# Optimization experiments

Hardware: AMD Instinct MI355X
Metric: run time of the kernel (lower is better)

## Reference

```python
import jax, jax.numpy as jnp
import numpy as np

B, W, M = 16, 32, 512
NH, HALF, K, H = 64, 32, 8, 8
LK = W // 2               # long-conv kernel size
LOUT = W - 2 * (LK - 1)   # = 2 (dilated valid conv output length)
NSP = 10                  # n_spatial (hardcoded in module)
GC1_IN = (1 + LOUT) * K   # 24


def setup_inputs() -> dict:
    key = jax.random.key(0)
    ks = jax.random.split(key, 23)
    def n(k, shp, s=0.1):
        return jax.random.normal(k, shp, jnp.float32) * s
    return dict(
        x=jax.random.normal(ks[0], (B, W, M), jnp.float32),
        adj=jax.random.uniform(ks[1], (M, M), jnp.float32) / M,  # row-normalized-ish dense adj
        Wih=n(ks[2], (NH, 1)), Whh=n(ks[3], (NH, NH)),
        bih=n(ks[4], (NH,)), bhh=n(ks[5], (NH,)),
        W1=n(ks[6], (HALF, NH)), W2=n(ks[7], (HALF, NH)), b1=n(ks[8], (HALF,)),
        V=n(ks[9], (HALF,)), bv=n(ks[10], (1,)),
        Wb=n(ks[11], (M, M)), wb=n(ks[12], (1,)),
        conv_w=n(ks[13], (K, 1, W)), conv_b=n(ks[14], (K,)),
        convl_w=n(ks[15], (K, 1, LK)), convl_b=n(ks[16], (K,)),
        gc1_w=n(ks[17], (GC1_IN, NH)), gc1_b=n(ks[18], (NH,)),
        gc2_w=n(ks[19], (NH, NSP)), gc2_b=n(ks[20], (NSP,)),
        out_w=n(ks[21], (H, NSP + NH)), out_b=n(ks[22], (H,)),
    )


def reference(x, adj, Wih, Whh, bih, bhh, W1, W2, b1, V, bv, Wb, wb,
              conv_w, conv_b, convl_w, convl_b, gc1_w, gc1_b, gc2_w, gc2_b,
              out_w, out_b):
    b = x.shape[0]
    # [b, w, m] -> per-node sequences [b*m, w]
    seq = jnp.transpose(x, (0, 2, 1)).reshape(b * M, W)

    # vanilla tanh RNN, input_size=1 (batched over all b*m series)
    inp = seq[:, :, None] * Wih[:, 0] + (bih + bhh)          # [b*m, w, nh]
    def step(h, it):
        return jnp.tanh(it + h @ Whh.T), None
    h0 = jnp.zeros((b * M, NH), x.dtype)
    last_hid, _ = jax.lax.scan(step, h0, jnp.swapaxes(inp, 0, 1))
    last_hid = last_hid.reshape(b, M, NH)                    # out_temporal

    # pairwise additive attention: a[b,i,j] = V . elu(W1 h_j + W2 h_i + b1) + bv
    e1 = last_hid @ W1.T                                     # [b, m, half] (j role)
    e2 = last_hid @ W2.T                                     # [b, m, half] (i role)
    a = jax.nn.elu(e2[:, :, None, :] + e1[:, None, :, :] + b1)  # [b,m,m,half]
    a_mx = a @ V + bv                                        # [b, m, m]
    # F.normalize(p=2, dim=1)
    norm = jnp.sqrt(jnp.sum(a_mx * a_mx, axis=1, keepdims=True))
    a_mx = a_mx / jnp.maximum(norm, 1e-12)

    # per-node short conv (kernel == window -> out len 1) as a single matmul
    r_short = seq @ conv_w[:, 0, :].T + conv_b               # [b*m, k]
    # per-node dilated long conv, batched over all b*m series
    r_long = jax.lax.conv_general_dilated(
        seq[:, None, :], convl_w, window_strides=(1,), padding='VALID',
        rhs_dilation=(2,), dimension_numbers=('NCW', 'OIW', 'NCW'))
    r_long = r_long + convl_b[None, :, None]                 # [b*m, k, LOUT]
    r = jnp.concatenate([r_short[:, :, None], r_long], axis=-1)  # [b*m, k, 1+LOUT]
    r = jax.nn.relu(r.reshape(b, M, GC1_IN))

    # gated mix of static normalized adj and learned attention adj
    c = jax.nn.sigmoid(a_mx @ Wb + wb)
    adj_mix = adj[None] * c + a_mx * (1.0 - c)               # [b, m, m]

    # two dense graph conv layers: relu(adj @ (h @ W) + b)
    h1 = jax.nn.relu(adj_mix @ (r @ gc1_w) + gc1_b)          # [b, m, nh]
    out_spatial = jax.nn.relu(adj_mix @ (h1 @ gc2_w) + gc2_b)  # [b, m, nsp]

    feat = jnp.concatenate([out_spatial, last_hid], axis=-1)  # [b, m, nsp+nh]
    out = feat @ out_w.T + out_b                              # [b, m, h]
    return jnp.transpose(out, (0, 2, 1))                      # [b, h, m]
```

## Files before the change

### kernel.cpp

```cpp
#include <hip/hip_runtime.h>


typedef __attribute__((ext_vector_type(8))) short bf16x8;
typedef __attribute__((ext_vector_type(4))) float f32x4;
#define MFMA16 __builtin_amdgcn_mfma_f32_16x16x32_bf16

__device__ __forceinline__ unsigned short f2bf(float f) {
    unsigned u = __float_as_uint(f);
    u += 0x7fff + ((u >> 16) & 1);
    return (unsigned short)(u >> 16);
}
__device__ __forceinline__ float bf2f(unsigned short h) {
    return __uint_as_float(((unsigned)h) << 16);
}
__device__ __forceinline__ float fast_tanh(float x) {
    float e = __expf(2.f * x);
    return 1.f - 2.f / (e + 1.f);
}

__global__ __launch_bounds__(256) void fused1_kernel(
    const float* __restrict__ x, const float* __restrict__ Wih,
    const float* __restrict__ Whh, const float* __restrict__ bih,
    const float* __restrict__ bhh, const float* __restrict__ W1,
    const float* __restrict__ W2, float* __restrict__ lh,
    float* __restrict__ e1, float* __restrict__ e2,
    const float* __restrict__ conv_w, const float* __restrict__ conv_b,
    const float* __restrict__ convl_w, const float* __restrict__ convl_b,
    const float* __restrict__ gc1_w, unsigned short* __restrict__ rgT,
    const float* __restrict__ Wb, unsigned short* __restrict__ WbT,
    float* __restrict__ nrmss)
{
    __shared__ __align__(16) char smem[17408];
    int blk = blockIdx.x, t = threadIdx.x;

    if (blk < 128) {
        int wid = t >> 6, lane = t & 63;
        int l15 = lane & 15, quad = lane >> 4;
        int rowblk = blk * 64;
        int row0 = rowblk + wid * 16;
        int b = rowblk >> 9, mb = rowblk & 511;
        float* xs = (float*)smem;
        unsigned short* hs = (unsigned short*)(smem + 8192);

        bf16x8 afr[4][2];
#pragma unroll
        for (int mt = 0; mt < 4; ++mt)
#pragma unroll
            for (int hf = 0; hf < 2; ++hf) {
                const float* src = Whh + (16 * mt + l15) * 64 + 32 * hf + quad * 8;
                union { bf16x8 v; unsigned short u[8]; } tmp;
#pragma unroll
                for (int j = 0; j < 8; ++j) tmp.u[j] = f2bf(src[j]);
                afr[mt][hf] = tmp.v;
            }
        bf16x8 wfr[2][2][2];
#pragma unroll
        for (int e = 0; e < 2; ++e)
#pragma unroll
            for (int nt = 0; nt < 2; ++nt)
#pragma unroll
                for (int kf = 0; kf < 2; ++kf) {
                    const float* Wsrc = (e ? W2 : W1);
                    const float* src = Wsrc + (16 * nt + l15) * 64 + 32 * kf + quad * 8;
                    union { bf16x8 v; unsigned short u[8]; } tmp;
#pragma unroll
                    for (int j = 0; j < 8; ++j) tmp.u[j] = f2bf(src[j]);
                    wfr[e][nt][kf] = tmp.v;
                }
        float wihv[4][4], bsv[4][4];
#pragma unroll
        for (int mt = 0; mt < 4; ++mt)
#pragma unroll
            for (int r = 0; r < 4; ++r) {
                int n = 16 * mt + quad * 4 + r;
                wihv[mt][r] = Wih[n];
                bsv[mt][r]  = bih[n] + bhh[n];
            }

        for (int u = t; u < 2048; u += 256) {
            int tt = u >> 6, c = u & 63;
            xs[tt * 64 + c] = x[(b * 32 + tt) * 512 + mb + c];
        }
        for (int u = lane; u < 1152; u += 64) hs[wid * 1152 + u] = 0;
        __syncthreads();

        int mloc = wid * 16;
        unsigned short* hw0 = hs + wid * 1152;
        float th[4][4];
        for (int tstep = 0; tstep < 32; ++tstep) {
            bf16x8 b0 = *(bf16x8*)(hw0 + l15 * 72 + quad * 8);
            bf16x8 b1 = *(bf16x8*)(hw0 + l15 * 72 + 32 + quad * 8);
            float xt = xs[tstep * 64 + mloc + l15];
            f32x4 acc[4];
#pragma unroll
            for (int mt = 0; mt < 4; ++mt) {
                f32x4 z = {0.f, 0.f, 0.f, 0.f};
                acc[mt] = MFMA16(afr[mt][0], b0, z, 0, 0, 0);
                acc[mt] = MFMA16(afr[mt][1], b1, acc[mt], 0, 0, 0);
            }
#pragma unroll
            for (int mt = 0; mt < 4; ++mt) {
                ushort4 hwv;
#pragma unroll
                for (int r = 0; r < 4; ++r)
                    th[mt][r] = fast_tanh(acc[mt][r] + xt * wihv[mt][r] + bsv[mt][r]);
                hwv.x = f2bf(th[mt][0]); hwv.y = f2bf(th[mt][1]);
                hwv.z = f2bf(th[mt][2]); hwv.w = f2bf(th[mt][3]);
                *(ushort4*)(hw0 + l15 * 72 + 16 * mt + quad * 4) = hwv;
            }
        }
#pragma unroll
        for (int mt = 0; mt < 4; ++mt)
            *(float4*)(lh + (row0 + l15) * 64 + 16 * mt + quad * 4) =
                make_float4(th[mt][0], th[mt][1], th[mt][2], th[mt][3]);

        bf16x8 a0 = *(bf16x8*)(hw0 + l15 * 72 + quad * 8);
        bf16x8 a1 = *(bf16x8*)(hw0 + l15 * 72 + 32 + quad * 8);
#pragma unroll
        for (int e = 0; e < 2; ++e) {
            float* dst = e ? e2 : e1;
#pragma unroll
            for (int nt = 0; nt < 2; ++nt) {
                f32x4 z = {0.f, 0.f, 0.f, 0.f};
                f32x4 ee = MFMA16(a0, wfr[e][nt][0], z, 0, 0, 0);
                ee = MFMA16(a1, wfr[e][nt][1], ee, 0, 0, 0);
#pragma unroll
                for (int r = 0; r < 4; ++r)
                    dst[(row0 + quad * 4 + r) * 32 + 16 * nt + l15] = ee[r];
            }
        }
    } else if (blk < 384) {
        int blk2 = blk - 128;
        int r0 = blk2 * 32;
        int bb = r0 >> 9, m0 = r0 & 511;
        float* xs  = (float*)smem;
        float* rrs = (float*)(smem + 4096);
        for (int u = t; u < 1024; u += 256) {
            int w = u >> 5, mm = u & 31;
            xs[u] = x[(bb * 32 + w) * 512 + m0 + mm];
        }
        __syncthreads();
        {
            int k = t & 7, rl = t >> 3;
            float s = conv_b[k];
            for (int w = 0; w < 32; ++w) s += xs[w * 32 + rl] * conv_w[k * 32 + w];
            float l0 = convl_b[k], l1 = l0;
            for (int tt = 0; tt < 16; ++tt) {
                float wv = convl_w[k * 16 + tt];
                l0 += xs[(2 * tt) * 32 + rl] * wv;
                l1 += xs[(2 * tt + 1) * 32 + rl] * wv;
            }
            rrs[rl * 25 + k * 3 + 0] = fmaxf(s, 0.f);
            rrs[rl * 25 + k * 3 + 1] = fmaxf(l0, 0.f);
            rrs[rl * 25 + k * 3 + 2] = fmaxf(l1, 0.f);
        }
        __syncthreads();
        int rl = t & 31, nb = t >> 5;
#pragma unroll
        for (int q = 0; q < 8; ++q) {
            int n = nb * 8 + q;
            float acc = 0.f;
#pragma unroll
            for (int c = 0; c < 24; ++c) acc += rrs[rl * 25 + c] * gc1_w[c * 64 + n];
            rgT[bb * 32768 + n * 512 + m0 + rl] = f2bf(acc);
        }
    } else if (blk < 640) {
        int bid = blk - 384;
        int nb = (bid & 15) * 32, kb = (bid >> 4) * 32;
        float* tile = (float*)smem;
        for (int u = t; u < 1024; u += 256) {
            int r = u >> 5, c = u & 31;
            tile[r * 33 + c] = Wb[(kb + r) * 512 + nb + c];
        }
        __syncthreads();
        for (int u = t; u < 1024; u += 256) {
            int r = u >> 5, c = u & 31;
            WbT[(nb + r) * 512 + kb + c] = f2bf(tile[c * 33 + r]);
        }
    } else {
        nrmss[(blk - 640) * 256 + t] = 0.f;
    }
}

__global__ __launch_bounds__(256) void amx_kernel(
    const float* __restrict__ e1, const float* __restrict__ e2,
    const float* __restrict__ b1p, const float* __restrict__ Vp,
    const float* __restrict__ bvp, unsigned short* __restrict__ amxb,
    float* __restrict__ nrmss)
{
    int bb = blockIdx.z;
    int i0 = blockIdx.y * 64, j0 = blockIdx.x * 64;
    __shared__ float e2s[64][33], e1s[64][33];
    __shared__ float Vs[32];
    __shared__ float red[16][68];
    int t = threadIdx.x;
    for (int u = t; u < 2048; u += 256) {
        int r = u >> 5, c = u & 31;
        e2s[r][c] = e2[(bb * 512 + i0 + r) * 32 + c];
        e1s[r][c] = e1[(bb * 512 + j0 + r) * 32 + c] + b1p[c];
    }
    if (t < 32) Vs[t] = Vp[t];
    __syncthreads();
    int ti = (t >> 4) * 4, tj = (t & 15) * 4;
    float acc[4][4] = {};
#pragma unroll
    for (int h = 0; h < 32; ++h) {
        float vv = Vs[h];
        float xi[4], yj[4], Exi[4], Eyj[4];
#pragma unroll
        for (int p = 0; p < 4; ++p) { xi[p] = e2s[ti + p][h]; Exi[p] = __expf(xi[p]); }
#pragma unroll
        for (int q = 0; q < 4; ++q) { yj[q] = e1s[tj + q][h]; Eyj[q] = __expf(yj[q]); }
#pragma unroll
        for (int p = 0; p < 4; ++p)
#pragma unroll
            for (int q = 0; q < 4; ++q) {
                float v = xi[p] + yj[q];
                float prod = Exi[p] * Eyj[q];
                float el = v > 0.f ? v : prod - 1.f;
                acc[p][q] += vv * el;
            }
    }
    float bv = bvp[0];
    float ss[4] = {0.f, 0.f, 0.f, 0.f};
#pragma unroll
    for (int p = 0; p < 4; ++p) {
        float v0 = acc[p][0] + bv, v1 = acc[p][1] + bv;
        float v2 = acc[p][2] + bv, v3 = acc[p][3] + bv;
        ushort4 o;
        o.x = f2bf(v0); o.y = f2bf(v1); o.z = f2bf(v2); o.w = f2bf(v3);
        *(ushort4*)(amxb + (bb * 512 + i0 + ti + p) * 512 + j0 + tj) = o;
        ss[0] += v0 * v0; ss[1] += v1 * v1; ss[2] += v2 * v2; ss[3] += v3 * v3;
    }
#pragma unroll
    for (int q = 0; q < 4; ++q) red[t >> 4][tj + q] = ss[q];
    __syncthreads();
    if (t < 64) {
        float s = 0.f;
#pragma unroll
        for (int g = 0; g < 16; ++g) s += red[g][t];
        atomicAdd(&nrmss[bb * 512 + j0 + t], s);
    }
}

__global__ __launch_bounds__(256) void gemm_adjmix(
    const unsigned short* __restrict__ amxb, const unsigned short* __restrict__ WbT,
    const float* __restrict__ wbp, const float* __restrict__ adj,
    const float* __restrict__ nrmss, unsigned short* __restrict__ adjmix)
{
    int bb = blockIdx.z;
    int i0 = blockIdx.y * 64, j0 = blockIdx.x * 64;
    __shared__ __align__(16) short As[64 * 72];
    __shared__ __align__(16) short Bs[64 * 72];
    __shared__ float rn[512];
    int t = threadIdx.x, w = t >> 6, lane = t & 63;
    int l15 = lane & 15, quad = lane >> 4;
    for (int u = t; u < 512; u += 256)
        rn[u] = 1.f / fmaxf(sqrtf(nrmss[bb * 512 + u]), 1e-12f);
    const unsigned short* Ag = amxb + bb * 262144;
    f32x4 acc[4] = {};
    for (int kk = 1; kk <= 8; ++kk) {
        int k0 = (j0 + 64 * kk) & 511;
        __syncthreads();
#pragma unroll
        for (int u0 = 0; u0 < 2; ++u0) {
            int u = t + u0 * 256;
            int i = u >> 3, o = u & 7;
            *(int4*)(Bs + i * 72 + o * 8) =
                *(const int4*)(WbT + (j0 + i) * 512 + k0 + o * 8);
            union { int4 v; unsigned short us[8]; } ur;
            ur.v = *(const int4*)(Ag + (i0 + i) * 512 + k0 + o * 8);
            union { int4 v; unsigned short us[8]; } ow;
#pragma unroll
            for (int c = 0; c < 8; ++c)
                ow.us[c] = f2bf(bf2f(ur.us[c]) * rn[k0 + o * 8 + c]);
            *(int4*)(As + i * 72 + o * 8) = ow.v;
        }
        __syncthreads();
        bf16x8 a0 = *(bf16x8*)(As + (16 * w + l15) * 72 + quad * 8);
        bf16x8 a1 = *(bf16x8*)(As + (16 * w + l15) * 72 + 32 + quad * 8);
#pragma unroll
        for (int nt = 0; nt < 4; ++nt) {
            bf16x8 b0 = *(bf16x8*)(Bs + (16 * nt + l15) * 72 + quad * 8);
            bf16x8 b1 = *(bf16x8*)(Bs + (16 * nt + l15) * 72 + 32 + quad * 8);
            acc[nt] = MFMA16(a0, b0, acc[nt], 0, 0, 0);
            acc[nt] = MFMA16(a1, b1, acc[nt], 0, 0, 0);
        }
    }
    float wb = wbp[0];
#pragma unroll
    for (int nt = 0; nt < 4; ++nt)
#pragma unroll
    for (int r = 0; r < 4; ++r) {
        int il = 16 * w + quad * 4 + r;
        int jl = 16 * nt + l15;
        int i = i0 + il, j = j0 + jl;
        float s  = acc[nt][r] + wb;
        float cv = 1.f / (1.f + __expf(-s));
        float am = bf2f((unsigned short)As[il * 72 + jl]);
        float ad = adj[i * 512 + j];
        adjmix[(bb * 512 + i) * 512 + j] = f2bf(ad * cv + am * (1.f - cv));
    }
}

__global__ __launch_bounds__(256) void gemm_h1(
    const unsigned short* __restrict__ adjmix, const unsigned short* __restrict__ rgT,
    const float* __restrict__ gc1_b, const float* __restrict__ gc2_w,
    float* __restrict__ h1g)
{
    int bb = blockIdx.y;
    int i0 = blockIdx.x * 32;
    __shared__ __align__(16) short As[32 * 72];
    __shared__ __align__(16) short Bs[64 * 72];
    __shared__ float h1s[32][72];
    int t = threadIdx.x, w = t >> 6, lane = t & 63;
    int l15 = lane & 15, quad = lane >> 4;
    int rt = w & 1, ntb = (w >> 1) * 2;
    const unsigned short* Ag = adjmix + bb * 262144;
    const unsigned short* Bg = rgT + bb * 32768;
    f32x4 acc[2] = {};
    for (int k0 = 0; k0 < 512; k0 += 64) {
        __syncthreads();
        {
            int i = t >> 3, o = t & 7;
            *(int4*)(As + i * 72 + o * 8) =
                *(const int4*)(Ag + (i0 + i) * 512 + k0 + o * 8);
        }
#pragma unroll
        for (int u0 = 0; u0 < 2; ++u0) {
            int u = t + u0 * 256;
            int i = u >> 3, o = u & 7;
            *(int4*)(Bs + i * 72 + o * 8) =
                *(const int4*)(Bg + i * 512 + k0 + o * 8);
        }
        __syncthreads();
        bf16x8 a0 = *(bf16x8*)(As + (16 * rt + l15) * 72 + quad * 8);
        bf16x8 a1 = *(bf16x8*)(As + (16 * rt + l15) * 72 + 32 + quad * 8);
#pragma unroll
        for (int q = 0; q < 2; ++q) {
            int nt = ntb + q;
            bf16x8 b0 = *(bf16x8*)(Bs + (16 * nt + l15) * 72 + quad * 8);
            bf16x8 b1 = *(bf16x8*)(Bs + (16 * nt + l15) * 72 + 32 + quad * 8);
            acc[q] = MFMA16(a0, b0, acc[q], 0, 0, 0);
            acc[q] = MFMA16(a1, b1, acc[q], 0, 0, 0);
        }
    }
#pragma unroll
    for (int q = 0; q < 2; ++q)
#pragma unroll
    for (int r = 0; r < 4; ++r) {
        int il = 16 * rt + quad * 4 + r;
        int j = 16 * (ntb + q) + l15;
        h1s[il][j] = fmaxf(acc[q][r] + gc1_b[j], 0.f);
    }
    __syncthreads();
    for (int u = t; u < 320; u += 256) {
        int row = u / 10, ns = u - row * 10;
        float a2 = 0.f;
#pragma unroll
        for (int j = 0; j < 64; ++j) a2 += h1s[row][j] * gc2_w[j * 10 + ns];
        h1g[(bb * 512 + i0 + row) * 10 + ns] = a2;
    }
}

__global__ __launch_bounds__(256) void ospout_kernel(
    const unsigned short* __restrict__ adjmix, const float* __restrict__ h1g,
    const float* __restrict__ gc2_b, const float* __restrict__ lh,
    const float* __restrict__ out_w, const float* __restrict__ out_b,
    float* __restrict__ out)
{
    int r0 = blockIdx.x * 8;
    int bb = r0 >> 9;
    int wid = threadIdx.x >> 6, lane = threadIdx.x & 63;
    __shared__ float Bsm[10][512];
    __shared__ float ow[8][80];
    __shared__ float ob[8], g2b[10];
    for (int u = threadIdx.x; u < 5120; u += 256) {
        int k = u / 10, ns = u - k * 10;
        Bsm[ns][k] = h1g[bb * 5120 + u];
    }
    if (threadIdx.x < 8)  ob[threadIdx.x]  = out_b[threadIdx.x];
    if (threadIdx.x < 10) g2b[threadIdx.x] = gc2_b[threadIdx.x];
    for (int u = threadIdx.x; u < 592; u += 256) {
        int hh = u / 74, c = u - hh * 74;
        ow[hh][c] = out_w[u];
    }
    __syncthreads();
#pragma unroll
    for (int half = 0; half < 2; ++half) {
        int row = r0 + half * 4 + wid, m = row & 511;
        const unsigned short* Ar = adjmix + row * 512;
        float a[8];
#pragma unroll
        for (int q = 0; q < 8; ++q) a[q] = bf2f(Ar[lane + 64 * q]);
        float os[10];
#pragma unroll
        for (int ns = 0; ns < 10; ++ns) {
            float s = 0.f;
#pragma unroll
            for (int q = 0; q < 8; ++q) s += a[q] * Bsm[ns][lane + 64 * q];
#pragma unroll
            for (int off = 32; off; off >>= 1) s += __shfl_xor(s, off);
            os[ns] = fmaxf(s + g2b[ns], 0.f);
        }
        float lv = lh[row * 64 + lane];
#pragma unroll
        for (int hh = 0; hh < 8; ++hh) {
            float t1 = lv * ow[hh][10 + lane];
#pragma unroll
            for (int off = 32; off; off >>= 1) t1 += __shfl_xor(t1, off);
            if (lane == hh) {
                float acc = ob[hh] + t1;
#pragma unroll
                for (int ns = 0; ns < 10; ++ns) acc += os[ns] * ow[hh][ns];
                out[bb * 4096 + hh * 512 + m] = acc;
            }
        }
    }
}

extern "C" void kernel_launch(void* const* d_in, const int* in_sizes, int n_in,
                              void* d_out, int out_size, void* d_ws, size_t ws_size,
                              hipStream_t stream)
{
    const float* x       = (const float*)d_in[0];
    const float* adj     = (const float*)d_in[1];
    const float* Wih     = (const float*)d_in[2];
    const float* Whh     = (const float*)d_in[3];
    const float* bih     = (const float*)d_in[4];
    const float* bhh     = (const float*)d_in[5];
    const float* W1      = (const float*)d_in[6];
    const float* W2      = (const float*)d_in[7];
    const float* b1      = (const float*)d_in[8];
    const float* V       = (const float*)d_in[9];
    const float* bv      = (const float*)d_in[10];
    const float* Wb      = (const float*)d_in[11];
    const float* wb      = (const float*)d_in[12];
    const float* conv_w  = (const float*)d_in[13];
    const float* conv_b  = (const float*)d_in[14];
    const float* convl_w = (const float*)d_in[15];
    const float* convl_b = (const float*)d_in[16];
    const float* gc1_w   = (const float*)d_in[17];
    const float* gc1_b   = (const float*)d_in[18];
    const float* gc2_w   = (const float*)d_in[19];
    const float* gc2_b   = (const float*)d_in[20];
    const float* out_w   = (const float*)d_in[21];
    const float* out_b   = (const float*)d_in[22];

    float* ws    = (float*)d_ws;
    float* lh    = ws;
    float* e1    = lh + 524288;
    float* e2    = e1 + 262144;
    float* nrmss = e2 + 262144;
    float* h1g   = nrmss + 8192;
    unsigned short* amxb    = (unsigned short*)(h1g + 81920);
    unsigned short* adjmixb = amxb + 4194304;
    unsigned short* WbT     = adjmixb + 4194304;
    unsigned short* rgT     = WbT + 262144;

    fused1_kernel<<<672, 256, 0, stream>>>(
        x, Wih, Whh, bih, bhh, W1, W2, lh, e1, e2,
        conv_w, conv_b, convl_w, convl_b, gc1_w, rgT, Wb, WbT, nrmss);
    amx_kernel<<<dim3(8, 8, 16), 256, 0, stream>>>(e1, e2, b1, V, bv,
                                                   amxb, nrmss);
    gemm_adjmix<<<dim3(8, 8, 16), 256, 0, stream>>>(amxb, WbT, wb, adj,
                                                    nrmss, adjmixb);
    gemm_h1<<<dim3(16, 16), 256, 0, stream>>>(adjmixb, rgT, gc1_b, gc2_w, h1g);
    ospout_kernel<<<1024, 256, 0, stream>>>(adjmixb, h1g, gc2_b, lh,
                                            out_w, out_b, (float*)d_out);
}
```

Baseline: 206.4 us.

## Co-schedule RNN and conv branches in one block; halve ospout grid

```diff
diff --git a/kernel.cpp b/kernel.cpp
--- a/kernel.cpp
+++ b/kernel.cpp
@@ -30,142 +30,140 @@
     const float* __restrict__ Wb, unsigned short* __restrict__ WbT,
     float* __restrict__ nrmss)
 {
-    __shared__ __align__(16) char smem[17408];
+    __shared__ __align__(16) char smem[12160];
     int blk = blockIdx.x, t = threadIdx.x;
 
-    if (blk < 128) {
+    if (blk < 256) {
         int wid = t >> 6, lane = t & 63;
-        int l15 = lane & 15, quad = lane >> 4;
-        int rowblk = blk * 64;
-        int row0 = rowblk + wid * 16;
+        int rowblk = blk * 32;
         int b = rowblk >> 9, mb = rowblk & 511;
         float* xs = (float*)smem;
-        unsigned short* hs = (unsigned short*)(smem + 8192);
-
-        bf16x8 afr[4][2];
-#pragma unroll
-        for (int mt = 0; mt < 4; ++mt)
-#pragma unroll
-            for (int hf = 0; hf < 2; ++hf) {
-                const float* src = Whh + (16 * mt + l15) * 64 + 32 * hf + quad * 8;
-                union { bf16x8 v; unsigned short u[8]; } tmp;
-#pragma unroll
-                for (int j = 0; j < 8; ++j) tmp.u[j] = f2bf(src[j]);
-                afr[mt][hf] = tmp.v;
-            }
-        bf16x8 wfr[2][2][2];
-#pragma unroll
-        for (int e = 0; e < 2; ++e)
-#pragma unroll
-            for (int nt = 0; nt < 2; ++nt)
-#pragma unroll
-                for (int kf = 0; kf < 2; ++kf) {
-                    const float* Wsrc = (e ? W2 : W1);
-                    const float* src = Wsrc + (16 * nt + l15) * 64 + 32 * kf + quad * 8;
+        unsigned short* hs = (unsigned short*)(smem + 4096);
+        float* rrs = (float*)(smem + 8704);
+
+        for (int u = t; u < 1024; u += 256) {
+            int tt = u >> 5, c = u & 31;
+            xs[tt * 32 + c] = x[(b * 32 + tt) * 512 + mb + c];
+        }
+        for (int u = t; u < 2304; u += 256) hs[u] = 0;
+        __syncthreads();
+
+        if (wid < 2) {
+            int l15 = lane & 15, quad = lane >> 4;
+            int row0 = rowblk + wid * 16;
+            unsigned short* hw0 = hs + wid * 1152;
+
+            bf16x8 afr[4][2];
+#pragma unroll
+            for (int mt = 0; mt < 4; ++mt)
+#pragma unroll
+                for (int hf = 0; hf < 2; ++hf) {
+                    const float* src = Whh + (16 * mt + l15) * 64 + 32 * hf + quad * 8;
                     union { bf16x8 v; unsigned short u[8]; } tmp;
 #pragma unroll
                     for (int j = 0; j < 8; ++j) tmp.u[j] = f2bf(src[j]);
-                    wfr[e][nt][kf] = tmp.v;
-                }
-        float wihv[4][4], bsv[4][4];
-#pragma unroll
-        for (int mt = 0; mt < 4; ++mt)
-#pragma unroll
-            for (int r = 0; r < 4; ++r) {
-                int n = 16 * mt + quad * 4 + r;
-                wihv[mt][r] = Wih[n];
-                bsv[mt][r]  = bih[n] + bhh[n];
-            }
-
-        for (int u = t; u < 2048; u += 256) {
-            int tt = u >> 6, c = u & 63;
-            xs[tt * 64 + c] = x[(b * 32 + tt) * 512 + mb + c];
-        }
-        for (int u = lane; u < 1152; u += 64) hs[wid * 1152 + u] = 0;
-        __syncthreads();
-
-        int mloc = wid * 16;
-        unsigned short* hw0 = hs + wid * 1152;
-        float th[4][4];
-        for (int tstep = 0; tstep < 32; ++tstep) {
-            bf16x8 b0 = *(bf16x8*)(hw0 + l15 * 72 + quad * 8);
-            bf16x8 b1 = *(bf16x8*)(hw0 + l15 * 72 + 32 + quad * 8);
-            float xt = xs[tstep * 64 + mloc + l15];
-            f32x4 acc[4];
-#pragma unroll
-            for (int mt = 0; mt < 4; ++mt) {
-                f32x4 z = {0.f, 0.f, 0.f, 0.f};
-                acc[mt] = MFMA16(afr[mt][0], b0, z, 0, 0, 0);
-                acc[mt] = MFMA16(afr[mt][1], b1, acc[mt], 0, 0, 0);
-            }
-#pragma unroll
-            for (int mt = 0; mt < 4; ++mt) {
-                ushort4 hwv;
-#pragma unroll
-                for (int r = 0; r < 4; ++r)
-                    th[mt][r] = fast_tanh(acc[mt][r] + xt * wihv[mt][r] + bsv[mt][r]);
-                hwv.x = f2bf(th[mt][0]); hwv.y = f2bf(th[mt][1]);
-                hwv.z = f2bf(th[mt][2]); hwv.w = f2bf(th[mt][3]);
-                *(ushort4*)(hw0 + l15 * 72 + 16 * mt + quad * 4) = hwv;
-            }
-        }
-#pragma unroll
-        for (int mt = 0; mt < 4; ++mt)
-            *(float4*)(lh + (row0 + l15) * 64 + 16 * mt + quad * 4) =
-                make_float4(th[mt][0], th[mt][1], th[mt][2], th[mt][3]);
-
-        bf16x8 a0 = *(bf16x8*)(hw0 + l15 * 72 + quad * 8);
-        bf16x8 a1 = *(bf16x8*)(hw0 + l15 * 72 + 32 + quad * 8);
-#pragma unroll
-        for (int e = 0; e < 2; ++e) {
-            float* dst = e ? e2 : e1;
-#pragma unroll
-            for (int nt = 0; nt < 2; ++nt) {
-                f32x4 z = {0.f, 0.f, 0.f, 0.f};
-                f32x4 ee = MFMA16(a0, wfr[e][nt][0], z, 0, 0, 0);
-                ee = MFMA16(a1, wfr[e][nt][1], ee, 0, 0, 0);
-#pragma unroll
-                for (int r = 0; r < 4; ++r)
-                    dst[(row0 + quad * 4 + r) * 32 + 16 * nt + l15] = ee[r];
-            }
-        }
-    } else if (blk < 384) {
-        int blk2 = blk - 128;
-        int r0 = blk2 * 32;
-        int bb = r0 >> 9, m0 = r0 & 511;
-        float* xs  = (float*)smem;
-        float* rrs = (float*)(smem + 4096);
-        for (int u = t; u < 1024; u += 256) {
-            int w = u >> 5, mm = u & 31;
-            xs[u] = x[(bb * 32 + w) * 512 + m0 + mm];
-        }
-        __syncthreads();
-        {
-            int k = t & 7, rl = t >> 3;
-            float s = conv_b[k];
-            for (int w = 0; w < 32; ++w) s += xs[w * 32 + rl] * conv_w[k * 32 + w];
-            float l0 = convl_b[k], l1 = l0;
-            for (int tt = 0; tt < 16; ++tt) {
-                float wv = convl_w[k * 16 + tt];
-                l0 += xs[(2 * tt) * 32 + rl] * wv;
-                l1 += xs[(2 * tt + 1) * 32 + rl] * wv;
-            }
-            rrs[rl * 25 + k * 3 + 0] = fmaxf(s, 0.f);
-            rrs[rl * 25 + k * 3 + 1] = fmaxf(l0, 0.f);
-            rrs[rl * 25 + k * 3 + 2] = fmaxf(l1, 0.f);
-        }
-        __syncthreads();
-        int rl = t & 31, nb = t >> 5;
-#pragma unroll
-        for (int q = 0; q < 8; ++q) {
-            int n = nb * 8 + q;
-            float acc = 0.f;
-#pragma unroll
-            for (int c = 0; c < 24; ++c) acc += rrs[rl * 25 + c] * gc1_w[c * 64 + n];
-            rgT[bb * 32768 + n * 512 + m0 + rl] = f2bf(acc);
-        }
-    } else if (blk < 640) {
-        int bid = blk - 384;
+                    afr[mt][hf] = tmp.v;
+                }
+            bf16x8 wfr[2][2][2];
+#pragma unroll
+            for (int e = 0; e < 2; ++e)
+#pragma unroll
+                for (int nt = 0; nt < 2; ++nt)
+#pragma unroll
+                    for (int kf = 0; kf < 2; ++kf) {
+                        const float* Wsrc = (e ? W2 : W1);
+                        const float* src = Wsrc + (16 * nt + l15) * 64 + 32 * kf + quad * 8;
+                        union { bf16x8 v; unsigned short u[8]; } tmp;
+#pragma unroll
+                        for (int j = 0; j < 8; ++j) tmp.u[j] = f2bf(src[j]);
+                        wfr[e][nt][kf] = tmp.v;
+                    }
+            float wihv[4][4], bsv[4][4];
+#pragma unroll
+            for (int mt = 0; mt < 4; ++mt)
+#pragma unroll
+                for (int r = 0; r < 4; ++r) {
+                    int n = 16 * mt + quad * 4 + r;
+                    wihv[mt][r] = Wih[n];
+                    bsv[mt][r]  = bih[n] + bhh[n];
+                }
+
+            float th[4][4];
+            for (int tstep = 0; tstep < 32; ++tstep) {
+                bf16x8 b0 = *(bf16x8*)(hw0 + l15 * 72 + quad * 8);
+                bf16x8 b1 = *(bf16x8*)(hw0 + l15 * 72 + 32 + quad * 8);
+                float xt = xs[tstep * 32 + wid * 16 + l15];
+                f32x4 acc[4];
+#pragma unroll
+                for (int mt = 0; mt < 4; ++mt) {
+                    f32x4 z = {0.f, 0.f, 0.f, 0.f};
+                    acc[mt] = MFMA16(afr[mt][0], b0, z, 0, 0, 0);
+                    acc[mt] = MFMA16(afr[mt][1], b1, acc[mt], 0, 0, 0);
+                }
+#pragma unroll
+                for (int mt = 0; mt < 4; ++mt) {
+                    ushort4 hwv;
+#pragma unroll
+                    for (int r = 0; r < 4; ++r)
+                        th[mt][r] = fast_tanh(acc[mt][r] + xt * wihv[mt][r] + bsv[mt][r]);
+                    hwv.x = f2bf(th[mt][0]); hwv.y = f2bf(th[mt][1]);
+                    hwv.z = f2bf(th[mt][2]); hwv.w = f2bf(th[mt][3]);
+                    *(ushort4*)(hw0 + l15 * 72 + 16 * mt + quad * 4) = hwv;
+                }
+            }
+#pragma unroll
+            for (int mt = 0; mt < 4; ++mt)
+                *(float4*)(lh + (row0 + l15) * 64 + 16 * mt + quad * 4) =
+                    make_float4(th[mt][0], th[mt][1], th[mt][2], th[mt][3]);
+
+            bf16x8 a0 = *(bf16x8*)(hw0 + l15 * 72 + quad * 8);
+            bf16x8 a1 = *(bf16x8*)(hw0 + l15 * 72 + 32 + quad * 8);
+#pragma unroll
+            for (int e = 0; e < 2; ++e) {
+                float* dst = e ? e2 : e1;
+#pragma unroll
+                for (int nt = 0; nt < 2; ++nt) {
+                    f32x4 z = {0.f, 0.f, 0.f, 0.f};
+                    f32x4 ee = MFMA16(a0, wfr[e][nt][0], z, 0, 0, 0);
+                    ee = MFMA16(a1, wfr[e][nt][1], ee, 0, 0, 0);
+#pragma unroll
+                    for (int r = 0; r < 4; ++r)
+                        dst[(row0 + quad * 4 + r) * 32 + 16 * nt + l15] = ee[r];
+                }
+            }
+        } else {
+            int wid2 = wid - 2;
+#pragma unroll
+            for (int rep = 0; rep < 2; ++rep) {
+                int task = rep * 64 + lane;
+                int rl = wid2 * 16 + (task >> 3);
+                int k  = task & 7;
+                float s = conv_b[k];
+                for (int w = 0; w < 32; ++w) s += xs[w * 32 + rl] * conv_w[k * 32 + w];
+                float l0 = convl_b[k], l1 = l0;
+                for (int tt = 0; tt < 16; ++tt) {
+                    float wv = convl_w[k * 16 + tt];
+                    l0 += xs[(2 * tt) * 32 + rl] * wv;
+                    l1 += xs[(2 * tt + 1) * 32 + rl] * wv;
+                }
+                rrs[rl * 25 + k * 3 + 0] = fmaxf(s, 0.f);
+                rrs[rl * 25 + k * 3 + 1] = fmaxf(l0, 0.f);
+                rrs[rl * 25 + k * 3 + 2] = fmaxf(l1, 0.f);
+            }
+            __builtin_amdgcn_wave_barrier();
+            int rl = wid2 * 16 + (lane & 15);
+            int nb = lane >> 4;
+#pragma unroll
+            for (int q = 0; q < 16; ++q) {
+                int n = nb * 16 + q;
+                float acc = 0.f;
+#pragma unroll
+                for (int c = 0; c < 24; ++c) acc += rrs[rl * 25 + c] * gc1_w[c * 64 + n];
+                rgT[b * 32768 + n * 512 + mb + rl] = f2bf(acc);
+            }
+        }
+    } else if (blk < 512) {
+        int bid = blk - 256;
         int nb = (bid & 15) * 32, kb = (bid >> 4) * 32;
         float* tile = (float*)smem;
         for (int u = t; u < 1024; u += 256) {
@@ -178,7 +176,7 @@
             WbT[(nb + r) * 512 + kb + c] = f2bf(tile[c * 33 + r]);
         }
     } else {
-        nrmss[(blk - 640) * 256 + t] = 0.f;
+        nrmss[(blk - 512) * 256 + t] = 0.f;
     }
 }
 
@@ -369,7 +367,7 @@
     const float* __restrict__ out_w, const float* __restrict__ out_b,
     float* __restrict__ out)
 {
-    int r0 = blockIdx.x * 8;
+    int r0 = blockIdx.x * 16;
     int bb = r0 >> 9;
     int wid = threadIdx.x >> 6, lane = threadIdx.x & 63;
     __shared__ float Bsm[10][512];
@@ -387,7 +385,7 @@
     }
     __syncthreads();
 #pragma unroll
-    for (int half = 0; half < 2; ++half) {
+    for (int half = 0; half < 4; ++half) {
         int row = r0 + half * 4 + wid, m = row & 511;
         const unsigned short* Ar = adjmix + row * 512;
         float a[8];
@@ -458,7 +456,7 @@
     unsigned short* WbT     = adjmixb + 4194304;
     unsigned short* rgT     = WbT + 262144;
 
-    fused1_kernel<<<672, 256, 0, stream>>>(
+    fused1_kernel<<<544, 256, 0, stream>>>(
         x, Wih, Whh, bih, bhh, W1, W2, lh, e1, e2,
         conv_w, conv_b, convl_w, convl_b, gc1_w, rgT, Wb, WbT, nrmss);
     amx_kernel<<<dim3(8, 8, 16), 256, 0, stream>>>(e1, e2, b1, V, bv,
@@ -466,6 +464,6 @@
     gemm_adjmix<<<dim3(8, 8, 16), 256, 0, stream>>>(amxb, WbT, wb, adj,
                                                     nrmss, adjmixb);
     gemm_h1<<<dim3(16, 16), 256, 0, stream>>>(adjmixb, rgT, gc1_b, gc2_w, h1g);
-    ospout_kernel<<<1024, 256, 0, stream>>>(adjmixb, h1g, gc2_b, lh,
-                                            out_w, out_b, (float*)d_out);
-}
+    ospout_kernel<<<512, 256, 0, stream>>>(adjmixb, h1g, gc2_b, lh,
+                                           out_w, out_b, (float*)d_out);
+}
```

New measurement: 207.1 us (median of 2 runs). About the same (+0.3%).
